# Kernel optimization log

Measured on AMD Instinct MI355X. Metric: run time of the kernel, lower is better.

Reference implementation:

```python
import jax, jax.numpy as jnp
import numpy as np

B, T, M, R_DIM, D_IN, H, D_OUT = 16384, 10, 8, 256, 16, 32, 1


def setup_inputs() -> dict:
    key = jax.random.key(0)
    ks = jax.random.split(key, 16)
    f = jax.random.normal
    return {
        "V": f(ks[0], (B, D_IN), dtype=jnp.float32),
        "increments": f(ks[1], (B, T, M), dtype=jnp.float32),
        "W1": f(ks[2], (H, D_IN), dtype=jnp.float32) * 0.1,
        "b1": f(ks[3], (H,), dtype=jnp.float32) * 0.1,
        "W2": f(ks[4], (R_DIM, H), dtype=jnp.float32) * 0.1,
        "b2": f(ks[5], (R_DIM,), dtype=jnp.float32) * 0.1,
        "rho1": f(ks[6], (1, 1), dtype=jnp.float32) * 0.05,
        "rho2": f(ks[7], (1, 1), dtype=jnp.float32) * 0.05,
        "rho3": f(ks[8], (1, 1), dtype=jnp.float32) * 0.05,
        "rho4": f(ks[9], (1, 1), dtype=jnp.float32) * 0.05,
        "B1": f(ks[10], (R_DIM, R_DIM), dtype=jnp.float32),
        "B2": f(ks[11], (M, R_DIM, R_DIM), dtype=jnp.float32),
        "lam1": f(ks[12], (R_DIM, 1), dtype=jnp.float32),
        "lam2": f(ks[13], (M, R_DIM, 1), dtype=jnp.float32),
        "Wro": f(ks[14], (T, D_OUT, R_DIM), dtype=jnp.float32) * 0.1,
        "bro": f(ks[15], (T, D_OUT), dtype=jnp.float32) * 0.1,
    }


def reference(V, increments, W1, b1, W2, b2, rho1, rho2, rho3, rho4, B1, B2, lam1, lam2, Wro, bro):
    act = jnp.tanh
    # initial condition NN: (B, d_in) -> (B, r, 1)
    h = act(V @ W1.T + b1)
    R0 = (h @ W2.T + b2)[:, :, None]
    # Brownian path: cumsum of increments, first point forced to 0 (as in torch code)
    Wp = jnp.cumsum(increments, axis=1)
    Wp = Wp.at[:, 0, :].set(0.0)
    dW = jnp.moveaxis(Wp[:, 1:] - Wp[:, :-1], 1, 0)  # (T-1, B, m)

    def step(Rp, dw):  # Rp: (B, r, 1), dw: (B, m)
        drift = act(rho1 * jnp.einsum('ij,bjk->bik', B1, Rp) + rho2 * lam1)
        diff = act(rho3 * jnp.einsum('mij,bjk->bmik', B2, Rp) + rho4 * lam2)  # (B,m,r,1)
        Rn = Rp + drift + jnp.sum(diff * dw[:, :, None, None], axis=1)
        return Rn, Rn

    _, Rs = jax.lax.scan(step, R0, dW)
    Rall = jnp.concatenate([R0[None], Rs], axis=0)      # (T, B, r, 1)
    Rall = jnp.moveaxis(Rall, 0, 1)                     # (B, T, r, 1)
    # per-timestep readouts: (B,T,r) x (T,out,r) -> (B,T,out)
    x = jnp.einsum('btr,tor->bto', Rall[..., 0], Wro) + bro
    return x.reshape(x.shape[0], -1, 1)
```

## Files before the change

### kernel.cpp

```cpp
#include <hip/hip_runtime.h>

#define RD 256
#define BT 64
#define NTH 512
#define T_STEPS 9

typedef __attribute__((ext_vector_type(8))) short short8;
typedef __attribute__((ext_vector_type(8))) _Float16 half8;
typedef __attribute__((ext_vector_type(4))) float f32x4;

__device__ __forceinline__ float tanh_from_2x(float z) {
  float e = __expf(z);
  float r = __builtin_amdgcn_rcpf(e + 1.0f);
  return __builtin_fmaf(-2.0f, r, 1.0f);
}
__device__ __forceinline__ f32x4 mfma16h(half8 a, half8 b, f32x4 c) {
  return __builtin_amdgcn_mfma_f32_16x16x32_f16(a, b, c, 0, 0, 0);
}
__device__ __forceinline__ unsigned pack2h(float a, float b) {
  unsigned short ua = __builtin_bit_cast(unsigned short, (_Float16)a);
  unsigned short ub = __builtin_bit_cast(unsigned short, (_Float16)b);
  return (unsigned)ua | ((unsigned)ub << 16);
}

__global__ __launch_bounds__(64) void prep_w(const float* __restrict__ B1,
                                             const float* __restrict__ B2,
                                             _Float16* __restrict__ Wh) {
  const int blk = blockIdx.x;
  const int w = blk >> 7, rem = blk & 127;
  const int Mt = rem >> 3, kk = rem & 7;
  const int l = threadIdx.x, c = l & 15, g = l >> 4;
  const float* src = (w == 0 ? B1 : B2 + (size_t)(w - 1) * RD * RD)
                     + (size_t)(Mt * 16 + c) * RD + kk * 32 + g * 8;
  _Float16* d = Wh + (size_t)(((w * 8 + kk) * 16 + Mt) * 512) + l * 8;
  #pragma unroll
  for (int i = 0; i < 8; ++i) d[i] = (_Float16)src[i];
}

__global__ __launch_bounds__(NTH, 2) void sde_main(
    const float* __restrict__ V, const float* __restrict__ inc,
    const float* __restrict__ W1, const float* __restrict__ b1,
    const float* __restrict__ W2, const float* __restrict__ b2,
    const float* __restrict__ rho1p, const float* __restrict__ rho2p,
    const float* __restrict__ rho3p, const float* __restrict__ rho4p,
    const float* __restrict__ lam1, const float* __restrict__ lam2,
    const float* __restrict__ Wro, const float* __restrict__ bro,
    const _Float16* __restrict__ Wh, float* __restrict__ out) {
  __shared__ short8 Bex[2048];
  __shared__ float dW_s[T_STEPS * 8 * BT];
  __shared__ float lam_e[9 * RD];
  __shared__ float ro_part[8 * BT];

  const int tid = threadIdx.x;
  const int wv = tid >> 6, l = tid & 63, c = l & 15, g = l >> 4;
  const int b_base = blockIdx.x * BT;
  const float sa1 = 2.0f * rho1p[0], sa3 = 2.0f * rho3p[0];

  float* W2s  = (float*)Bex;
  float* actT = lam_e;

  {
    const float4* s = (const float4*)W2;
    float4* d = (float4*)W2s;
    #pragma unroll
    for (int j = 0; j < 4; ++j) d[j * NTH + tid] = s[j * NTH + tid];
  }
  {
    const int b = tid & 63, h0 = (tid >> 6) << 2;
    const float* Vb = V + (size_t)(b_base + b) * 16;
    float v[16];
    #pragma unroll
    for (int k = 0; k < 16; ++k) v[k] = Vb[k];
    #pragma unroll
    for (int i = 0; i < 4; ++i) {
      const int h = h0 + i;
      float s = b1[h];
      #pragma unroll
      for (int k = 0; k < 16; ++k) s += v[k] * W1[h * 16 + k];
      actT[h * 64 + b] = tanh_from_2x(2.0f * s);
    }
  }
  {
    const int b = tid >> 3, m = tid & 7;
    const float* ib = inc + (size_t)(b_base + b) * 80 + m;
    dW_s[m * BT + b] = ib[0] + ib[8];
    #pragma unroll
    for (int t = 1; t < 9; ++t) dW_s[(t * 8 + m) * BT + b] = ib[(t + 1) * 8];
  }
  __syncthreads();

  float mast[2][4][4];
  #pragma unroll
  for (int mt = 0; mt < 2; ++mt)
    #pragma unroll
    for (int i = 0; i < 4; ++i) {
      const float bb = b2[32 * wv + 16 * mt + 4 * g + i];
      #pragma unroll
      for (int nt = 0; nt < 4; ++nt) mast[mt][nt][i] = bb;
    }
  #pragma unroll 4
  for (int h = 0; h < 32; ++h) {
    float a[4];
    #pragma unroll
    for (int nt = 0; nt < 4; ++nt) a[nt] = actT[h * 64 + nt * 16 + c];
    #pragma unroll
    for (int mt = 0; mt < 2; ++mt)
      #pragma unroll
      for (int i = 0; i < 4; ++i) {
        const float w2v = W2s[(32 * wv + 16 * mt + 4 * g + i) * 32 + h];
        #pragma unroll
        for (int nt = 0; nt < 4; ++nt) mast[mt][nt][i] += w2v * a[nt];
      }
  }

  auto partials = [&](int t) {
    float s[4] = {0.f, 0.f, 0.f, 0.f};
    #pragma unroll
    for (int mt = 0; mt < 2; ++mt)
      #pragma unroll
      for (int i = 0; i < 4; ++i) {
        const float wr = Wro[t * RD + 32 * wv + 16 * mt + 4 * g + i];
        #pragma unroll
        for (int nt = 0; nt < 4; ++nt) s[nt] += wr * mast[mt][nt][i];
      }
    #pragma unroll
    for (int nt = 0; nt < 4; ++nt) {
      s[nt] += __shfl_xor(s[nt], 16);
      s[nt] += __shfl_xor(s[nt], 32);
    }
    if (g == 0) {
      #pragma unroll
      for (int nt = 0; nt < 4; ++nt) ro_part[wv * BT + nt * 16 + c] = s[nt];
    }
  };

  auto write_ex = [&]() {
    #pragma unroll
    for (int mt = 0; mt < 2; ++mt) {
      const int gq = 2 * mt + (g >> 1);
      const int hb = g & 1;
      #pragma unroll
      for (int nt = 0; nt < 4; ++nt) {
        const int slot = (wv * 4 + gq) * 64 + nt * 16 + c;
        uint2 pk;
        pk.x = pack2h(mast[mt][nt][0], mast[mt][nt][1]);
        pk.y = pack2h(mast[mt][nt][2], mast[mt][nt][3]);
        *((uint2*)((char*)&Bex[slot] + hb * 8)) = pk;
      }
    }
  };

  partials(0);
  __syncthreads();
  {
    const float rb2 = 2.0f * rho2p[0], rb4 = 2.0f * rho4p[0];
    for (int j = tid; j < 2304; j += NTH)
      lam_e[j] = (j < 256) ? rb2 * lam1[j] : rb4 * lam2[j - 256];
  }
  if (tid < BT) {
    float x = bro[0];
    #pragma unroll
    for (int q = 0; q < 8; ++q) x += ro_part[q * BT + tid];
    out[(size_t)(b_base + tid) * 10] = x;
  }
  write_ex();
  __syncthreads();

  const _Float16* pA0 = Wh + 2 * wv * 512 + l * 8;

  for (int t = 0; t < T_STEPS; ++t) {
    half8 Breg[8][4];
    #pragma unroll
    for (int kk = 0; kk < 8; ++kk)
      #pragma unroll
      for (int nt = 0; nt < 4; ++nt)
        Breg[kk][nt] = __builtin_bit_cast(
            half8, Bex[(kk * 4 + g) * 64 + nt * 16 + c]);

    half8 Ab[2][2];
    Ab[0][0] = *(const half8*)(pA0);
    Ab[0][1] = *(const half8*)(pA0 + 512);
    Ab[1][0] = *(const half8*)(pA0 + 8192);
    Ab[1][1] = *(const half8*)(pA0 + 8192 + 512);
    const _Float16* pPre = pA0 + 2 * 8192;

    #pragma unroll 1
    for (int w = 0; w < 9; ++w) {
      f32x4 acc[2][4];
      const f32x4 zero = {0.f, 0.f, 0.f, 0.f};
      #pragma unroll
      for (int mt = 0; mt < 2; ++mt)
        #pragma unroll
        for (int nt = 0; nt < 4; ++nt) acc[mt][nt] = zero;

      #pragma unroll
      for (int kk = 0; kk < 8; ++kk) {
        const int cur = kk & 1;
        #pragma unroll
        for (int mt = 0; mt < 2; ++mt)
          #pragma unroll
          for (int nt = 0; nt < 4; ++nt)
            acc[mt][nt] = mfma16h(Ab[cur][mt], Breg[kk][nt], acc[mt][nt]);
        if (w * 8 + kk + 2 < 72) {
          Ab[cur][0] = *(const half8*)(pPre);
          Ab[cur][1] = *(const half8*)(pPre + 512);
          pPre += 8192;
        }
      }

      const float sA = (w == 0) ? sa1 : sa3;
      float coef[4];
      if (w == 0) {
        coef[0] = 1.0f; coef[1] = 1.0f; coef[2] = 1.0f; coef[3] = 1.0f;
      } else {
        #pragma unroll
        for (int nt = 0; nt < 4; ++nt)
          coef[nt] = dW_s[((t * 8) + (w - 1)) * BT + nt * 16 + c];
      }
      #pragma unroll
      for (int mt = 0; mt < 2; ++mt)
        #pragma unroll
        for (int i = 0; i < 4; ++i) {
          const float le = lam_e[w * RD + 32 * wv + 16 * mt + 4 * g + i];
          #pragma unroll
          for (int nt = 0; nt < 4; ++nt) {
            const float th = tanh_from_2x(__builtin_fmaf(sA, acc[mt][nt][i], le));
            mast[mt][nt][i] = __builtin_fmaf(coef[nt], th, mast[mt][nt][i]);
          }
        }
    }

    partials(t + 1);
    __syncthreads();
    if (tid < BT) {
      float x = bro[t + 1];
      #pragma unroll
      for (int q = 0; q < 8; ++q) x += ro_part[q * BT + tid];
      out[(size_t)(b_base + tid) * 10 + (t + 1)] = x;
    }
    if (t < T_STEPS - 1) write_ex();
    __syncthreads();
  }
}

extern "C" void kernel_launch(void* const* d_in, const int* in_sizes, int n_in,
                              void* d_out, int out_size, void* d_ws, size_t ws_size,
                              hipStream_t stream) {
  const float* V    = (const float*)d_in[0];
  const float* inc  = (const float*)d_in[1];
  const float* W1   = (const float*)d_in[2];
  const float* b1   = (const float*)d_in[3];
  const float* W2   = (const float*)d_in[4];
  const float* b2   = (const float*)d_in[5];
  const float* rho1 = (const float*)d_in[6];
  const float* rho2 = (const float*)d_in[7];
  const float* rho3 = (const float*)d_in[8];
  const float* rho4 = (const float*)d_in[9];
  const float* B1   = (const float*)d_in[10];
  const float* B2   = (const float*)d_in[11];
  const float* lam1 = (const float*)d_in[12];
  const float* lam2 = (const float*)d_in[13];
  const float* Wro  = (const float*)d_in[14];
  const float* bro  = (const float*)d_in[15];
  float* out = (float*)d_out;

  _Float16* Wh = (_Float16*)d_ws;

  const int B = in_sizes[0] / 16;

  prep_w<<<9 * 16 * 8, 64, 0, stream>>>(B1, B2, Wh);
  sde_main<<<B / BT, NTH, 0, stream>>>(V, inc, W1, b1, W2, b2,
                                       rho1, rho2, rho3, rho4,
                                       lam1, lam2, Wro, bro, Wh, out);
}
```

Before: 294.4 us.

## Software-pipeline tanh epilogue with next weight slot's MFMAs via double accumulators

Restructures the per-timestep loop over the nine weight slots so the tanh/accumulate epilogue of one slot is interleaved with the MFMA chain of the next. It does this with two alternating accumulator sets and a four-deep A-operand prefetch ring. It also folds log2(e) into the rho and lambda scale factors so tanh can use a raw exp2, and packs to fp16 with cvt_pkrtz. The aim is to hide transcendental ALU latency behind matrix work. The cost is more register pressure under a tight launch bound, and unconditional prefetch loads that read past the end of the weight buffer on the final slot.

New measurement: 564.1 us. 91.6% more time.

```diff
diff --git a/kernel.cpp b/kernel.cpp
--- a/kernel.cpp
+++ b/kernel.cpp
@@ -7,21 +7,34 @@
 
 typedef __attribute__((ext_vector_type(8))) short short8;
 typedef __attribute__((ext_vector_type(8))) _Float16 half8;
+typedef __attribute__((ext_vector_type(2))) _Float16 half2v;
 typedef __attribute__((ext_vector_type(4))) float f32x4;
 
-__device__ __forceinline__ float tanh_from_2x(float z) {
-  float e = __expf(z);
+#if __has_builtin(__builtin_amdgcn_exp2f)
+#define EXP2(x) __builtin_amdgcn_exp2f(x)
+#else
+#define EXP2(x) exp2f(x)
+#endif
+
+__device__ __forceinline__ float tanh_plain(float x) {
+  float e = __expf(2.0f * x);
   float r = __builtin_amdgcn_rcpf(e + 1.0f);
   return __builtin_fmaf(-2.0f, r, 1.0f);
 }
 __device__ __forceinline__ f32x4 mfma16h(half8 a, half8 b, f32x4 c) {
   return __builtin_amdgcn_mfma_f32_16x16x32_f16(a, b, c, 0, 0, 0);
 }
+#if __has_builtin(__builtin_amdgcn_cvt_pkrtz)
+__device__ __forceinline__ unsigned pack2h(float a, float b) {
+  return __builtin_bit_cast(unsigned, __builtin_amdgcn_cvt_pkrtz(a, b));
+}
+#else
 __device__ __forceinline__ unsigned pack2h(float a, float b) {
   unsigned short ua = __builtin_bit_cast(unsigned short, (_Float16)a);
   unsigned short ub = __builtin_bit_cast(unsigned short, (_Float16)b);
   return (unsigned)ua | ((unsigned)ub << 16);
 }
+#endif
 
 __global__ __launch_bounds__(64) void prep_w(const float* __restrict__ B1,
                                              const float* __restrict__ B2,
@@ -35,6 +48,42 @@
   _Float16* d = Wh + (size_t)(((w * 8 + kk) * 16 + Mt) * 512) + l * 8;
   #pragma unroll
   for (int i = 0; i < 8; ++i) d[i] = (_Float16)src[i];
+}
+
+template <bool DOEPI>
+__device__ __forceinline__ void slot_run(
+    f32x4 (&acc)[2][4], f32x4 (&pacc)[2][4], half8 (&Ab)[4][2],
+    const half8 (&Breg)[8][4], const _Float16*& pPre,
+    float (&mast)[2][4][4], float sA2p, const float (&coefp)[4],
+    const float (&lep)[8]) {
+  const f32x4 zero = {0.f, 0.f, 0.f, 0.f};
+  #pragma unroll
+  for (int mt = 0; mt < 2; ++mt)
+    #pragma unroll
+    for (int nt = 0; nt < 4; ++nt) acc[mt][nt] = zero;
+
+  #pragma unroll
+  for (int kk = 0; kk < 8; ++kk) {
+    const int cur = kk & 3;
+    #pragma unroll
+    for (int nt = 0; nt < 4; ++nt) {
+      acc[0][nt] = mfma16h(Ab[cur][0], Breg[kk][nt], acc[0][nt]);
+      acc[1][nt] = mfma16h(Ab[cur][1], Breg[kk][nt], acc[1][nt]);
+    }
+    if (DOEPI) {
+      #pragma unroll
+      for (int e = kk * 4; e < kk * 4 + 4; ++e) {
+        const int mt_ = e >> 4, nt_ = (e >> 2) & 3, i_ = e & 3;
+        const float z = __builtin_fmaf(sA2p, pacc[mt_][nt_][i_], lep[mt_ * 4 + i_]);
+        const float r = __builtin_amdgcn_rcpf(EXP2(z) + 1.0f);
+        const float th = __builtin_fmaf(-2.0f, r, 1.0f);
+        mast[mt_][nt_][i_] = __builtin_fmaf(coefp[nt_], th, mast[mt_][nt_][i_]);
+      }
+    }
+    Ab[cur][0] = *(const half8*)(pPre);
+    Ab[cur][1] = *(const half8*)(pPre + 512);
+    pPre += 8192;
+  }
 }
 
 __global__ __launch_bounds__(NTH, 2) void sde_main(
@@ -54,7 +103,9 @@
   const int tid = threadIdx.x;
   const int wv = tid >> 6, l = tid & 63, c = l & 15, g = l >> 4;
   const int b_base = blockIdx.x * BT;
-  const float sa1 = 2.0f * rho1p[0], sa3 = 2.0f * rho3p[0];
+  const float LOG2E = 1.4426950408889634f;
+  const float sa1_2 = 2.0f * LOG2E * rho1p[0];
+  const float sa3_2 = 2.0f * LOG2E * rho3p[0];
 
   float* W2s  = (float*)Bex;
   float* actT = lam_e;
@@ -77,7 +128,7 @@
       float s = b1[h];
       #pragma unroll
       for (int k = 0; k < 16; ++k) s += v[k] * W1[h * 16 + k];
-      actT[h * 64 + b] = tanh_from_2x(2.0f * s);
+      actT[h * 64 + b] = tanh_plain(s);
     }
   }
   {
@@ -153,7 +204,7 @@
   partials(0);
   __syncthreads();
   {
-    const float rb2 = 2.0f * rho2p[0], rb4 = 2.0f * rho4p[0];
+    const float rb2 = 2.0f * LOG2E * rho2p[0], rb4 = 2.0f * LOG2E * rho4p[0];
     for (int j = tid; j < 2304; j += NTH)
       lam_e[j] = (j < 256) ? rb2 * lam1[j] : rb4 * lam2[j - 256];
   }
@@ -167,6 +218,7 @@
   __syncthreads();
 
   const _Float16* pA0 = Wh + 2 * wv * 512 + l * 8;
+  const float ones[4] = {1.0f, 1.0f, 1.0f, 1.0f};
 
   for (int t = 0; t < T_STEPS; ++t) {
     half8 Breg[8][4];
@@ -177,57 +229,75 @@
         Breg[kk][nt] = __builtin_bit_cast(
             half8, Bex[(kk * 4 + g) * 64 + nt * 16 + c]);
 
-    half8 Ab[2][2];
-    Ab[0][0] = *(const half8*)(pA0);
-    Ab[0][1] = *(const half8*)(pA0 + 512);
-    Ab[1][0] = *(const half8*)(pA0 + 8192);
-    Ab[1][1] = *(const half8*)(pA0 + 8192 + 512);
-    const _Float16* pPre = pA0 + 2 * 8192;
+    half8 Ab[4][2];
+    const _Float16* pPre = pA0;
+    #pragma unroll
+    for (int d = 0; d < 4; ++d) {
+      Ab[d][0] = *(const half8*)(pPre);
+      Ab[d][1] = *(const half8*)(pPre + 512);
+      pPre += 8192;
+    }
+
+    f32x4 accA[2][4], accB[2][4];
+    float lepz[8];
+    #pragma unroll
+    for (int q = 0; q < 8; ++q) lepz[q] = 0.f;
+
+    slot_run<false>(accA, accB, Ab, Breg, pPre, mast, 0.f, ones, lepz);
 
     #pragma unroll 1
-    for (int w = 0; w < 9; ++w) {
-      f32x4 acc[2][4];
-      const f32x4 zero = {0.f, 0.f, 0.f, 0.f};
-      #pragma unroll
-      for (int mt = 0; mt < 2; ++mt)
-        #pragma unroll
-        for (int nt = 0; nt < 4; ++nt) acc[mt][nt] = zero;
-
-      #pragma unroll
-      for (int kk = 0; kk < 8; ++kk) {
-        const int cur = kk & 1;
-        #pragma unroll
-        for (int mt = 0; mt < 2; ++mt)
+    for (int p = 0; p < 4; ++p) {
+      {
+        const int pv = 2 * p;
+        float coefp[4], lep[8];
+        float sA2p;
+        if (pv == 0) {
+          sA2p = sa1_2;
+          #pragma unroll
+          for (int nt = 0; nt < 4; ++nt) coefp[nt] = 1.0f;
+        } else {
+          sA2p = sa3_2;
           #pragma unroll
           for (int nt = 0; nt < 4; ++nt)
-            acc[mt][nt] = mfma16h(Ab[cur][mt], Breg[kk][nt], acc[mt][nt]);
-        if (w * 8 + kk + 2 < 72) {
-          Ab[cur][0] = *(const half8*)(pPre);
-          Ab[cur][1] = *(const half8*)(pPre + 512);
-          pPre += 8192;
+            coefp[nt] = dW_s[(t * 8 + pv - 1) * BT + nt * 16 + c];
         }
-      }
-
-      const float sA = (w == 0) ? sa1 : sa3;
-      float coef[4];
-      if (w == 0) {
-        coef[0] = 1.0f; coef[1] = 1.0f; coef[2] = 1.0f; coef[3] = 1.0f;
-      } else {
+        const float4 l0 = *(const float4*)&lam_e[pv * RD + 32 * wv + 4 * g];
+        const float4 l1 = *(const float4*)&lam_e[pv * RD + 32 * wv + 16 + 4 * g];
+        lep[0] = l0.x; lep[1] = l0.y; lep[2] = l0.z; lep[3] = l0.w;
+        lep[4] = l1.x; lep[5] = l1.y; lep[6] = l1.z; lep[7] = l1.w;
+        slot_run<true>(accB, accA, Ab, Breg, pPre, mast, sA2p, coefp, lep);
+      }
+      {
+        const int pv = 2 * p + 1;
+        float coefp[4], lep[8];
         #pragma unroll
         for (int nt = 0; nt < 4; ++nt)
-          coef[nt] = dW_s[((t * 8) + (w - 1)) * BT + nt * 16 + c];
-      }
-      #pragma unroll
-      for (int mt = 0; mt < 2; ++mt)
-        #pragma unroll
-        for (int i = 0; i < 4; ++i) {
-          const float le = lam_e[w * RD + 32 * wv + 16 * mt + 4 * g + i];
-          #pragma unroll
-          for (int nt = 0; nt < 4; ++nt) {
-            const float th = tanh_from_2x(__builtin_fmaf(sA, acc[mt][nt][i], le));
-            mast[mt][nt][i] = __builtin_fmaf(coef[nt], th, mast[mt][nt][i]);
-          }
-        }
+          coefp[nt] = dW_s[(t * 8 + pv - 1) * BT + nt * 16 + c];
+        const float4 l0 = *(const float4*)&lam_e[pv * RD + 32 * wv + 4 * g];
+        const float4 l1 = *(const float4*)&lam_e[pv * RD + 32 * wv + 16 + 4 * g];
+        lep[0] = l0.x; lep[1] = l0.y; lep[2] = l0.z; lep[3] = l0.w;
+        lep[4] = l1.x; lep[5] = l1.y; lep[6] = l1.z; lep[7] = l1.w;
+        slot_run<true>(accA, accB, Ab, Breg, pPre, mast, sa3_2, coefp, lep);
+      }
+    }
+
+    {
+      float coefp[4], lep[8];
+      #pragma unroll
+      for (int nt = 0; nt < 4; ++nt)
+        coefp[nt] = dW_s[(t * 8 + 7) * BT + nt * 16 + c];
+      const float4 l0 = *(const float4*)&lam_e[8 * RD + 32 * wv + 4 * g];
+      const float4 l1 = *(const float4*)&lam_e[8 * RD + 32 * wv + 16 + 4 * g];
+      lep[0] = l0.x; lep[1] = l0.y; lep[2] = l0.z; lep[3] = l0.w;
+      lep[4] = l1.x; lep[5] = l1.y; lep[6] = l1.z; lep[7] = l1.w;
+      #pragma unroll
+      for (int e = 0; e < 32; ++e) {
+        const int mt_ = e >> 4, nt_ = (e >> 2) & 3, i_ = e & 3;
+        const float z = __builtin_fmaf(sa3_2, accA[mt_][nt_][i_], lep[mt_ * 4 + i_]);
+        const float r = __builtin_amdgcn_rcpf(EXP2(z) + 1.0f);
+        const float th = __builtin_fmaf(-2.0f, r, 1.0f);
+        mast[mt_][nt_][i_] = __builtin_fmaf(coefp[nt_], th, mast[mt_][nt_][i_]);
+      }
     }
 
     partials(t + 1);
```

## Software-pipeline tanh epilogue with MFMA slots and fold log2e into exp2

Applied to the files above, without the earlier changes.

Splits each weight matrix's work into two half-slots (mt=0/1) and interleaves the tanh/accumulate epilogue of the previous slot's accumulators with the MFMA issue of the current slot. The goal is to hide transcendental VALU work behind matrix ops instead of running it serially after all MFMAs. The change also folds log2(e) into the scale and bias constants so tanh can use the native exp2, and uses the packed round-toward-zero convert for fp16 packing. A single A-operand ring buffer of depth 4 replaces the double buffer. The cost is more complex control flow and higher register pressure. The round-toward-zero convert also changes fp16 rounding slightly.

After: 331.8 us. +12.7%, slower.

```diff
diff --git a/kernel.cpp b/kernel.cpp
--- a/kernel.cpp
+++ b/kernel.cpp
@@ -9,19 +9,31 @@
 typedef __attribute__((ext_vector_type(8))) _Float16 half8;
 typedef __attribute__((ext_vector_type(4))) float f32x4;
 
-__device__ __forceinline__ float tanh_from_2x(float z) {
-  float e = __expf(z);
+#if __has_builtin(__builtin_amdgcn_exp2f)
+#define EXP2(x) __builtin_amdgcn_exp2f(x)
+#else
+#define EXP2(x) exp2f(x)
+#endif
+
+__device__ __forceinline__ float tanh_plain(float x) {
+  float e = __expf(2.0f * x);
   float r = __builtin_amdgcn_rcpf(e + 1.0f);
   return __builtin_fmaf(-2.0f, r, 1.0f);
 }
 __device__ __forceinline__ f32x4 mfma16h(half8 a, half8 b, f32x4 c) {
   return __builtin_amdgcn_mfma_f32_16x16x32_f16(a, b, c, 0, 0, 0);
 }
+#if __has_builtin(__builtin_amdgcn_cvt_pkrtz)
+__device__ __forceinline__ unsigned pack2h(float a, float b) {
+  return __builtin_bit_cast(unsigned, __builtin_amdgcn_cvt_pkrtz(a, b));
+}
+#else
 __device__ __forceinline__ unsigned pack2h(float a, float b) {
   unsigned short ua = __builtin_bit_cast(unsigned short, (_Float16)a);
   unsigned short ub = __builtin_bit_cast(unsigned short, (_Float16)b);
   return (unsigned)ua | ((unsigned)ub << 16);
 }
+#endif
 
 __global__ __launch_bounds__(64) void prep_w(const float* __restrict__ B1,
                                              const float* __restrict__ B2,
@@ -35,6 +47,37 @@
   _Float16* d = Wh + (size_t)(((w * 8 + kk) * 16 + Mt) * 512) + l * 8;
   #pragma unroll
   for (int i = 0; i < 8; ++i) d[i] = (_Float16)src[i];
+}
+
+template <int H, bool DOEPI, int MTP>
+__device__ __forceinline__ void run_slot(
+    f32x4 (&acc)[4], const f32x4 (&pacc)[4], half8 (&Ab)[4],
+    const half8 (&Breg)[8][4], const _Float16* pw,
+    float (&mast)[2][4][4], float sA2, const float (&coef)[4],
+    const float (&lep)[4]) {
+  const f32x4 zero = {0.f, 0.f, 0.f, 0.f};
+  #pragma unroll
+  for (int kk = 0; kk < 8; ++kk) {
+    const half8 a = Ab[kk & 3];
+    #pragma unroll
+    for (int nt = 0; nt < 4; ++nt)
+      acc[nt] = mfma16h(a, Breg[kk][nt], (kk == 0) ? zero : acc[nt]);
+    if (DOEPI) {
+      const int nt_ = kk >> 1, i0 = (2 * kk) & 3, i1 = (2 * kk + 1) & 3;
+      const float z0 = __builtin_fmaf(sA2, pacc[nt_][i0], lep[i0]);
+      const float z1 = __builtin_fmaf(sA2, pacc[nt_][i1], lep[i1]);
+      const float r0 = __builtin_amdgcn_rcpf(EXP2(z0) + 1.0f);
+      const float r1 = __builtin_amdgcn_rcpf(EXP2(z1) + 1.0f);
+      const float t0 = __builtin_fmaf(-2.0f, r0, 1.0f);
+      const float t1 = __builtin_fmaf(-2.0f, r1, 1.0f);
+      mast[MTP][nt_][i0] = __builtin_fmaf(coef[nt_], t0, mast[MTP][nt_][i0]);
+      mast[MTP][nt_][i1] = __builtin_fmaf(coef[nt_], t1, mast[MTP][nt_][i1]);
+    }
+    const int off = (kk <= 4) ? ((kk + 3) * 8192 + H * 512)
+                              : (H == 0 ? (kk - 5) * 8192 + 512
+                                        : 65536 + (kk - 5) * 8192);
+    Ab[(kk + 3) & 3] = *(const half8*)(pw + off);
+  }
 }
 
 __global__ __launch_bounds__(NTH, 2) void sde_main(
@@ -54,7 +97,9 @@
   const int tid = threadIdx.x;
   const int wv = tid >> 6, l = tid & 63, c = l & 15, g = l >> 4;
   const int b_base = blockIdx.x * BT;
-  const float sa1 = 2.0f * rho1p[0], sa3 = 2.0f * rho3p[0];
+  const float LOG2E = 1.4426950408889634f;
+  const float sa1_2 = 2.0f * LOG2E * rho1p[0];
+  const float sa3_2 = 2.0f * LOG2E * rho3p[0];
 
   float* W2s  = (float*)Bex;
   float* actT = lam_e;
@@ -77,7 +122,7 @@
       float s = b1[h];
       #pragma unroll
       for (int k = 0; k < 16; ++k) s += v[k] * W1[h * 16 + k];
-      actT[h * 64 + b] = tanh_from_2x(2.0f * s);
+      actT[h * 64 + b] = tanh_plain(s);
     }
   }
   {
@@ -153,7 +198,7 @@
   partials(0);
   __syncthreads();
   {
-    const float rb2 = 2.0f * rho2p[0], rb4 = 2.0f * rho4p[0];
+    const float rb2 = 2.0f * LOG2E * rho2p[0], rb4 = 2.0f * LOG2E * rho4p[0];
     for (int j = tid; j < 2304; j += NTH)
       lam_e[j] = (j < 256) ? rb2 * lam1[j] : rb4 * lam2[j - 256];
   }
@@ -167,6 +212,8 @@
   __syncthreads();
 
   const _Float16* pA0 = Wh + 2 * wv * 512 + l * 8;
+  const float ones4[4] = {1.f, 1.f, 1.f, 1.f};
+  const float lep0[4] = {0.f, 0.f, 0.f, 0.f};
 
   for (int t = 0; t < T_STEPS; ++t) {
     half8 Breg[8][4];
@@ -177,57 +224,68 @@
         Breg[kk][nt] = __builtin_bit_cast(
             half8, Bex[(kk * 4 + g) * 64 + nt * 16 + c]);
 
-    half8 Ab[2][2];
-    Ab[0][0] = *(const half8*)(pA0);
-    Ab[0][1] = *(const half8*)(pA0 + 512);
-    Ab[1][0] = *(const half8*)(pA0 + 8192);
-    Ab[1][1] = *(const half8*)(pA0 + 8192 + 512);
-    const _Float16* pPre = pA0 + 2 * 8192;
+    half8 Ab[4];
+    Ab[0] = *(const half8*)(pA0);
+    Ab[1] = *(const half8*)(pA0 + 8192);
+    Ab[2] = *(const half8*)(pA0 + 16384);
+    const _Float16* pw = pA0;
+
+    f32x4 aX[4], aY[4];
+
+    run_slot<0, false, 0>(aX, aY, Ab, Breg, pw, mast, 0.f, ones4, lep0);
+    {
+      float lepA[4];
+      const float4 lv = *(const float4*)&lam_e[32 * wv + 4 * g];
+      lepA[0] = lv.x; lepA[1] = lv.y; lepA[2] = lv.z; lepA[3] = lv.w;
+      run_slot<1, true, 0>(aY, aX, Ab, Breg, pw, mast, sa1_2, ones4, lepA);
+    }
 
     #pragma unroll 1
-    for (int w = 0; w < 9; ++w) {
-      f32x4 acc[2][4];
-      const f32x4 zero = {0.f, 0.f, 0.f, 0.f};
-      #pragma unroll
-      for (int mt = 0; mt < 2; ++mt)
+    for (int w = 1; w < 9; ++w) {
+      pw += 65536;
+      {
+        const float sA2a = (w == 1) ? sa1_2 : sa3_2;
+        const int ia = (w == 1) ? 0 : (t * 8 + w - 2);
+        float coefA[4], lepB[4];
         #pragma unroll
-        for (int nt = 0; nt < 4; ++nt) acc[mt][nt] = zero;
-
-      #pragma unroll
-      for (int kk = 0; kk < 8; ++kk) {
-        const int cur = kk & 1;
-        #pragma unroll
-        for (int mt = 0; mt < 2; ++mt)
-          #pragma unroll
-          for (int nt = 0; nt < 4; ++nt)
-            acc[mt][nt] = mfma16h(Ab[cur][mt], Breg[kk][nt], acc[mt][nt]);
-        if (w * 8 + kk + 2 < 72) {
-          Ab[cur][0] = *(const half8*)(pPre);
-          Ab[cur][1] = *(const half8*)(pPre + 512);
-          pPre += 8192;
+        for (int nt = 0; nt < 4; ++nt) {
+          const float dv = dW_s[ia * BT + nt * 16 + c];
+          coefA[nt] = (w == 1) ? 1.0f : dv;
         }
-      }
-
-      const float sA = (w == 0) ? sa1 : sa3;
-      float coef[4];
-      if (w == 0) {
-        coef[0] = 1.0f; coef[1] = 1.0f; coef[2] = 1.0f; coef[3] = 1.0f;
-      } else {
+        const float4 lv = *(const float4*)&lam_e[(w - 1) * RD + 32 * wv + 16 + 4 * g];
+        lepB[0] = lv.x; lepB[1] = lv.y; lepB[2] = lv.z; lepB[3] = lv.w;
+        run_slot<0, true, 1>(aX, aY, Ab, Breg, pw, mast, sA2a, coefA, lepB);
+      }
+      {
+        float coefB[4], lepC[4];
         #pragma unroll
         for (int nt = 0; nt < 4; ++nt)
-          coef[nt] = dW_s[((t * 8) + (w - 1)) * BT + nt * 16 + c];
-      }
-      #pragma unroll
-      for (int mt = 0; mt < 2; ++mt)
-        #pragma unroll
-        for (int i = 0; i < 4; ++i) {
-          const float le = lam_e[w * RD + 32 * wv + 16 * mt + 4 * g + i];
-          #pragma unroll
-          for (int nt = 0; nt < 4; ++nt) {
-            const float th = tanh_from_2x(__builtin_fmaf(sA, acc[mt][nt][i], le));
-            mast[mt][nt][i] = __builtin_fmaf(coef[nt], th, mast[mt][nt][i]);
-          }
-        }
+          coefB[nt] = dW_s[(t * 8 + w - 1) * BT + nt * 16 + c];
+        const float4 lv = *(const float4*)&lam_e[w * RD + 32 * wv + 4 * g];
+        lepC[0] = lv.x; lepC[1] = lv.y; lepC[2] = lv.z; lepC[3] = lv.w;
+        run_slot<1, true, 0>(aY, aX, Ab, Breg, pw, mast, sa3_2, coefB, lepC);
+      }
+    }
+
+    {
+      float coefF[4], lepF[4];
+      #pragma unroll
+      for (int nt = 0; nt < 4; ++nt)
+        coefF[nt] = dW_s[(t * 8 + 7) * BT + nt * 16 + c];
+      const float4 lv = *(const float4*)&lam_e[8 * RD + 32 * wv + 16 + 4 * g];
+      lepF[0] = lv.x; lepF[1] = lv.y; lepF[2] = lv.z; lepF[3] = lv.w;
+      #pragma unroll
+      for (int kk = 0; kk < 8; ++kk) {
+        const int nt_ = kk >> 1, i0 = (2 * kk) & 3, i1 = (2 * kk + 1) & 3;
+        const float z0 = __builtin_fmaf(sa3_2, aY[nt_][i0], lepF[i0]);
+        const float z1 = __builtin_fmaf(sa3_2, aY[nt_][i1], lepF[i1]);
+        const float r0 = __builtin_amdgcn_rcpf(EXP2(z0) + 1.0f);
+        const float r1 = __builtin_amdgcn_rcpf(EXP2(z1) + 1.0f);
+        const float t0 = __builtin_fmaf(-2.0f, r0, 1.0f);
+        const float t1 = __builtin_fmaf(-2.0f, r1, 1.0f);
+        mast[1][nt_][i0] = __builtin_fmaf(coefF[nt_], t0, mast[1][nt_][i0]);
+        mast[1][nt_][i1] = __builtin_fmaf(coefF[nt_], t1, mast[1][nt_][i1]);
+      }
     }
 
     partials(t + 1);
```

## Stream B fragments from LDS per k-step and deepen A prefetch to eight stages

Applied to the files above, without the earlier changes.

The per-timestep 32-register B fragment cache is replaced by LDS reads per k-slice, which frees VGPRs for an eight-deep global prefetch ring of A fragments. The tanh is also changed to use raw v_exp_f32 with log2(e) folded into the scale constants. In addition, f16 packing uses cvt_pkrtz, and the lambda loads are vectorized to float4. The goal is to hide global load latency and cut VALU work, at the cost of more LDS traffic inside the MFMA loop. The prefetch also reads past the last needed slice on the final iterations, and round-toward-zero packing slightly changes numerics.

New measurement: 369.6 us. 1.26x slower.

```diff
diff --git a/kernel.cpp b/kernel.cpp
--- a/kernel.cpp
+++ b/kernel.cpp
@@ -9,19 +9,30 @@
 typedef __attribute__((ext_vector_type(8))) _Float16 half8;
 typedef __attribute__((ext_vector_type(4))) float f32x4;
 
-__device__ __forceinline__ float tanh_from_2x(float z) {
-  float e = __expf(z);
+__device__ __forceinline__ float exp_asm(float z) {
+  float e;
+  asm("v_exp_f32 %0, %1" : "=v"(e) : "v"(z));
+  return e;
+}
+__device__ __forceinline__ float tanh_plain(float x) {
+  float e = __expf(2.0f * x);
   float r = __builtin_amdgcn_rcpf(e + 1.0f);
   return __builtin_fmaf(-2.0f, r, 1.0f);
 }
 __device__ __forceinline__ f32x4 mfma16h(half8 a, half8 b, f32x4 c) {
   return __builtin_amdgcn_mfma_f32_16x16x32_f16(a, b, c, 0, 0, 0);
 }
+#if __has_builtin(__builtin_amdgcn_cvt_pkrtz)
+__device__ __forceinline__ unsigned pack2h(float a, float b) {
+  return __builtin_bit_cast(unsigned, __builtin_amdgcn_cvt_pkrtz(a, b));
+}
+#else
 __device__ __forceinline__ unsigned pack2h(float a, float b) {
   unsigned short ua = __builtin_bit_cast(unsigned short, (_Float16)a);
   unsigned short ub = __builtin_bit_cast(unsigned short, (_Float16)b);
   return (unsigned)ua | ((unsigned)ub << 16);
 }
+#endif
 
 __global__ __launch_bounds__(64) void prep_w(const float* __restrict__ B1,
                                              const float* __restrict__ B2,
@@ -54,7 +65,9 @@
   const int tid = threadIdx.x;
   const int wv = tid >> 6, l = tid & 63, c = l & 15, g = l >> 4;
   const int b_base = blockIdx.x * BT;
-  const float sa1 = 2.0f * rho1p[0], sa3 = 2.0f * rho3p[0];
+  const float LOG2E = 1.4426950408889634f;
+  const float sa1_2 = 2.0f * LOG2E * rho1p[0];
+  const float sa3_2 = 2.0f * LOG2E * rho3p[0];
 
   float* W2s  = (float*)Bex;
   float* actT = lam_e;
@@ -77,7 +90,7 @@
       float s = b1[h];
       #pragma unroll
       for (int k = 0; k < 16; ++k) s += v[k] * W1[h * 16 + k];
-      actT[h * 64 + b] = tanh_from_2x(2.0f * s);
+      actT[h * 64 + b] = tanh_plain(s);
     }
   }
   {
@@ -153,7 +166,7 @@
   partials(0);
   __syncthreads();
   {
-    const float rb2 = 2.0f * rho2p[0], rb4 = 2.0f * rho4p[0];
+    const float rb2 = 2.0f * LOG2E * rho2p[0], rb4 = 2.0f * LOG2E * rho4p[0];
     for (int j = tid; j < 2304; j += NTH)
       lam_e[j] = (j < 256) ? rb2 * lam1[j] : rb4 * lam2[j - 256];
   }
@@ -167,48 +180,41 @@
   __syncthreads();
 
   const _Float16* pA0 = Wh + 2 * wv * 512 + l * 8;
+  const char* BexB = (const char*)Bex;
+  const int vbyte = g * 1024 + c * 16;
+
+  f32x4 zero4 = {0.f, 0.f, 0.f, 0.f};
 
   for (int t = 0; t < T_STEPS; ++t) {
-    half8 Breg[8][4];
-    #pragma unroll
-    for (int kk = 0; kk < 8; ++kk)
-      #pragma unroll
-      for (int nt = 0; nt < 4; ++nt)
-        Breg[kk][nt] = __builtin_bit_cast(
-            half8, Bex[(kk * 4 + g) * 64 + nt * 16 + c]);
-
-    half8 Ab[2][2];
-    Ab[0][0] = *(const half8*)(pA0);
-    Ab[0][1] = *(const half8*)(pA0 + 512);
-    Ab[1][0] = *(const half8*)(pA0 + 8192);
-    Ab[1][1] = *(const half8*)(pA0 + 8192 + 512);
-    const _Float16* pPre = pA0 + 2 * 8192;
+    half8 Ab[8][2];
+    #pragma unroll
+    for (int s0 = 0; s0 < 8; ++s0) {
+      Ab[s0][0] = *(const half8*)(pA0 + s0 * 8192);
+      Ab[s0][1] = *(const half8*)(pA0 + s0 * 8192 + 512);
+    }
 
     #pragma unroll 1
     for (int w = 0; w < 9; ++w) {
       f32x4 acc[2][4];
-      const f32x4 zero = {0.f, 0.f, 0.f, 0.f};
-      #pragma unroll
-      for (int mt = 0; mt < 2; ++mt)
-        #pragma unroll
-        for (int nt = 0; nt < 4; ++nt) acc[mt][nt] = zero;
 
       #pragma unroll
       for (int kk = 0; kk < 8; ++kk) {
-        const int cur = kk & 1;
+        half8 Bf[4];
+        #pragma unroll
+        for (int nt = 0; nt < 4; ++nt)
+          Bf[nt] = *(const half8*)(BexB + vbyte + kk * 4096 + nt * 256);
         #pragma unroll
         for (int mt = 0; mt < 2; ++mt)
           #pragma unroll
           for (int nt = 0; nt < 4; ++nt)
-            acc[mt][nt] = mfma16h(Ab[cur][mt], Breg[kk][nt], acc[mt][nt]);
-        if (w * 8 + kk + 2 < 72) {
-          Ab[cur][0] = *(const half8*)(pPre);
-          Ab[cur][1] = *(const half8*)(pPre + 512);
-          pPre += 8192;
-        }
-      }
-
-      const float sA = (w == 0) ? sa1 : sa3;
+            acc[mt][nt] = mfma16h(Ab[kk][mt], Bf[nt],
+                                  (kk == 0) ? zero4 : acc[mt][nt]);
+        const _Float16* pn = pA0 + (size_t)(w * 8 + kk + 8) * 8192;
+        Ab[kk][0] = *(const half8*)(pn);
+        Ab[kk][1] = *(const half8*)(pn + 512);
+      }
+
+      const float sA2 = (w == 0) ? sa1_2 : sa3_2;
       float coef[4];
       if (w == 0) {
         coef[0] = 1.0f; coef[1] = 1.0f; coef[2] = 1.0f; coef[3] = 1.0f;
@@ -218,16 +224,20 @@
           coef[nt] = dW_s[((t * 8) + (w - 1)) * BT + nt * 16 + c];
       }
       #pragma unroll
-      for (int mt = 0; mt < 2; ++mt)
+      for (int mt = 0; mt < 2; ++mt) {
+        const float4 lv = *(const float4*)&lam_e[w * RD + 32 * wv + 16 * mt + 4 * g];
+        const float le[4] = {lv.x, lv.y, lv.z, lv.w};
         #pragma unroll
         for (int i = 0; i < 4; ++i) {
-          const float le = lam_e[w * RD + 32 * wv + 16 * mt + 4 * g + i];
           #pragma unroll
           for (int nt = 0; nt < 4; ++nt) {
-            const float th = tanh_from_2x(__builtin_fmaf(sA, acc[mt][nt][i], le));
+            const float z = __builtin_fmaf(sA2, acc[mt][nt][i], le[i]);
+            const float r = __builtin_amdgcn_rcpf(exp_asm(z) + 1.0f);
+            const float th = __builtin_fmaf(-2.0f, r, 1.0f);
             mast[mt][nt][i] = __builtin_fmaf(coef[nt], th, mast[mt][nt][i]);
           }
         }
+      }
     }
 
     partials(t + 1);
```
